# Kernel optimization log

Hardware: AMD Instinct MI355X
Metric: run time of the kernel (lower is better)

Reference implementation:

```python
import jax, jax.numpy as jnp
import numpy as np

C = 64
EPS_LN = 1e-5
EPS_BN = 1e-5


def _conv1x1(x, w, b):
    # x: (B,C,H,W), w: (O,I), b: (O,)
    return jnp.einsum('oi,bihw->bohw', w, x) + b[None, :, None, None]


def _cross_attn(x_a, x_b, wq, bq, wk, bk, wv, bv):
    # query from x_a, key/value from x_b; residual onto x_a
    b, c, h, w = x_a.shape
    hw = h * w
    scale = 1.0 / jnp.sqrt(jnp.asarray(C, x_a.dtype))
    q = _conv1x1(x_a, wq, bq).reshape(b, -1, hw)   # (B,C,HW)
    k = _conv1x1(x_b, wk, bk).reshape(b, -1, hw)   # (B,C,HW)
    v = _conv1x1(x_b, wv, bv).reshape(b, -1, hw)   # (B,C,HW)
    # torch: bmm(k^T, q) -> (B,HW,HW), softmax over last dim
    logits = jnp.einsum('bci,bcj->bij', k, q) * scale
    attn = jax.nn.softmax(logits, axis=-1)
    out = jnp.einsum('bci,bij->bcj', v, attn).reshape(b, -1, h, w)
    return out + x_a


def _layernorm_ch(x, g, b):
    # LayerNorm over channel dim of (B,C,H,W)
    mu = jnp.mean(x, axis=1, keepdims=True)
    var = jnp.var(x, axis=1, keepdims=True)
    xn = (x - mu) * jax.lax.rsqrt(var + EPS_LN)
    return xn * g[None, :, None, None] + b[None, :, None, None]


def setup_inputs() -> dict:
    key = jax.random.key(0)
    ks = jax.random.split(key, 20)
    B, H, W = 4, 64, 64
    s = 0.05
    d = {
        'x_s2': jax.random.normal(ks[0], (B, C, H, W), jnp.float32),
        'x_dem': jax.random.normal(ks[1], (B, C, H, W), jnp.float32),
        'wq1': jax.random.normal(ks[2], (C, C), jnp.float32) * s,
        'bq1': jnp.zeros((C,), jnp.float32),
        'wk1': jax.random.normal(ks[3], (C, C), jnp.float32) * s,
        'bk1': jnp.zeros((C,), jnp.float32),
        'wv1': jax.random.normal(ks[4], (C, C), jnp.float32) * s,
        'bv1': jnp.zeros((C,), jnp.float32),
        'wq2': jax.random.normal(ks[5], (C, C), jnp.float32) * s,
        'bq2': jnp.zeros((C,), jnp.float32),
        'wk2': jax.random.normal(ks[6], (C, C), jnp.float32) * s,
        'bk2': jnp.zeros((C,), jnp.float32),
        'wv2': jax.random.normal(ks[7], (C, C), jnp.float32) * s,
        'bv2': jnp.zeros((C,), jnp.float32),
        'ln_s2_w': jnp.ones((C,), jnp.float32),
        'ln_s2_b': jnp.zeros((C,), jnp.float32),
        'ln_dem_w': jnp.ones((C,), jnp.float32),
        'ln_dem_b': jnp.zeros((C,), jnp.float32),
        'fw1': jax.random.normal(ks[8], (C, 2 * C, 3, 3), jnp.float32) * s,
        'fb1': jnp.zeros((C,), jnp.float32),
        'bn_g': jnp.ones((C,), jnp.float32),
        'bn_b': jnp.zeros((C,), jnp.float32),
        'fw2': jax.random.normal(ks[9], (C, C), jnp.float32) * s,
        'fb2': jnp.zeros((C,), jnp.float32),
    }
    return d


def reference(x_s2, x_dem, wq1, bq1, wk1, bk1, wv1, bv1,
              wq2, bq2, wk2, bk2, wv2, bv2,
              ln_s2_w, ln_s2_b, ln_dem_w, ln_dem_b,
              fw1, fb1, bn_g, bn_b, fw2, fb2):
    out_s2 = _cross_attn(x_s2, x_dem, wq1, bq1, wk1, bk1, wv1, bv1)
    out_dem = _cross_attn(x_dem, x_s2, wq2, bq2, wk2, bk2, wv2, bv2)
    out_s2 = _layernorm_ch(out_s2, ln_s2_w, ln_s2_b)
    out_dem = _layernorm_ch(out_dem, ln_dem_w, ln_dem_b)
    combined = jnp.concatenate([out_s2, out_dem], axis=1)  # (B,2C,H,W)
    y = jax.lax.conv_general_dilated(
        combined, fw1, window_strides=(1, 1), padding='SAME',
        dimension_numbers=('NCHW', 'OIHW', 'NCHW')) + fb1[None, :, None, None]
    # BatchNorm2d in training mode: batch statistics over (B,H,W)
    mu = jnp.mean(y, axis=(0, 2, 3), keepdims=True)
    var = jnp.var(y, axis=(0, 2, 3), keepdims=True)
    y = (y - mu) * jax.lax.rsqrt(var + EPS_BN)
    y = y * bn_g[None, :, None, None] + bn_b[None, :, None, None]
    y = jax.nn.relu(y)
    return _conv1x1(y, fw2, fb2)
```

## Files before the change

### kernel.cpp

```cpp
#include <hip/hip_runtime.h>
#include <hip/hip_bf16.h>


using bf16x8 = __attribute__((ext_vector_type(8))) short;
using f32x4  = __attribute__((ext_vector_type(4))) float;
using f32x16 = __attribute__((ext_vector_type(16))) float;
typedef unsigned int uint2v __attribute__((ext_vector_type(2)));

#define MFMA16(a, b, c) __builtin_amdgcn_mfma_f32_16x16x32_bf16((a), (b), (c), 0, 0, 0)
#define MFMA32(a, b, c) __builtin_amdgcn_mfma_f32_32x32x16_bf16((a), (b), (c), 0, 0, 0)

constexpr int B_ = 4, C_ = 64, S_ = 4096;
constexpr float kQS = 0.18033688f;

constexpr size_t OFF_XT   = 0;
constexpr size_t OFF_WB   = 4u * 1024 * 1024;
constexpr size_t OFF_FW1R = OFF_WB + 64 * 1024;
constexpr size_t OFF_QT   = OFF_FW1R + 160 * 1024;
constexpr size_t OFF_KT   = OFF_QT + 4u * 1024 * 1024;
constexpr size_t OFF_V    = OFF_KT + 4u * 1024 * 1024;
constexpr size_t OFF_COMB = OFF_V + 4u * 1024 * 1024;
constexpr size_t OFF_Y    = OFF_COMB + 4u * 1024 * 1024;
constexpr size_t OFF_PART = OFF_Y + 4u * 1024 * 1024;
constexpr size_t OFF_BNA  = OFF_PART + 512 * 1024;
constexpr size_t OFF_BNB  = OFF_BNA + 1024;

__device__ __forceinline__ unsigned short f2bf(float f) {
  unsigned int u = __float_as_uint(f);
  unsigned int r = (u + 0x7fffu + ((u >> 16) & 1u)) >> 16;
  return (unsigned short)r;
}
__device__ __forceinline__ unsigned int cvt_pk_bf16(float lo, float hi) {
  unsigned int r;
  asm("v_cvt_pk_bf16_f32 %0, %1, %2" : "=v"(r) : "v"(lo), "v"(hi));
  return r;
}
__device__ __forceinline__ float fast_exp2(float x) {
#if __has_builtin(__builtin_amdgcn_exp2f)
  return __builtin_amdgcn_exp2f(x);
#else
  return exp2f(x);
#endif
}
__device__ __forceinline__ void plswap(unsigned int& a, unsigned int& b) {
  uint2v r = __builtin_amdgcn_permlane32_swap(a, b, false, false);
  a = r[0];
  b = r[1];
}

__device__ __forceinline__ void build_pv_frags(const f32x16 s, float& lsum,
                                               bf16x8* out) {
  float p[16];
#pragma unroll
  for (int r = 0; r < 16; ++r) p[r] = fast_exp2(s[r]);
  lsum += (((p[0] + p[1]) + (p[2] + p[3])) + ((p[4] + p[5]) + (p[6] + p[7]))) +
          (((p[8] + p[9]) + (p[10] + p[11])) + ((p[12] + p[13]) + (p[14] + p[15])));
#pragma unroll
  for (int h = 0; h < 2; ++h) {
    unsigned int X  = cvt_pk_bf16(p[8 * h + 0], p[8 * h + 1]);
    unsigned int X2 = cvt_pk_bf16(p[8 * h + 2], p[8 * h + 3]);
    unsigned int Y  = cvt_pk_bf16(p[8 * h + 4], p[8 * h + 5]);
    unsigned int Y2 = cvt_pk_bf16(p[8 * h + 6], p[8 * h + 7]);
    plswap(X, Y);
    plswap(X2, Y2);
    union { unsigned int u[4]; bf16x8 v; } bb;
    bb.u[0] = X; bb.u[1] = X2; bb.u[2] = Y; bb.u[3] = Y2;
    out[h] = bb.v;
  }
}

__global__ void k_prep(const float* wq1, const float* wk1, const float* wv1,
                       const float* wq2, const float* wk2, const float* wv2,
                       const float* fw2, const float* fw1,
                       const float* xs2, const float* xdem,
                       unsigned short* wb, unsigned short* fw1r,
                       unsigned short* xT) {
  __shared__ float lds[64][65];
  if (blockIdx.x < 400) {
    int g = blockIdx.x * 256 + threadIdx.x;
    if (g < 7 * 4096) {
      int m = g >> 12, idx = g & 4095;
      const float* src[7] = {wq1, wk1, wv1, wq2, wk2, wv2, fw2};
      float sc = (m == 0 || m == 3) ? kQS : 1.0f;
      wb[g] = f2bf(src[m][idx] * sc);
    } else {
      int t = g - 7 * 4096;
      if (t < 64 * 1152) {
        int o = t / 1152, kk = t % 1152;
        int dydx = kk >> 7, ci = kk & 127;
        fw1r[t] = f2bf(fw1[o * 1152 + ci * 9 + dydx]);
      }
    }
    return;
  }
  int bid = blockIdx.x - 400;
  int pt = bid & 63, b = (bid >> 6) & 3, tz = bid >> 8;
  int tid = threadIdx.x;
  const float* src = (tz == 0) ? xs2 : xdem;
  int p0 = pt * 64;
#pragma unroll
  for (int k = 0; k < 16; ++k) {
    int idx = k * 256 + tid;
    int c = idx >> 6, pp = idx & 63;
    lds[c][pp] = src[((size_t)(b * 64 + c) << 12) + p0 + pp];
  }
  __syncthreads();
  unsigned short* dst = xT + (size_t)tz * (B_ * S_ * C_);
#pragma unroll
  for (int k = 0; k < 4; ++k) {
    int p = (tid >> 4) + k * 16;
    int c0 = (tid & 15) * 4;
    ushort4 v;
    v.x = f2bf(lds[c0 + 0][p]);
    v.y = f2bf(lds[c0 + 1][p]);
    v.z = f2bf(lds[c0 + 2][p]);
    v.w = f2bf(lds[c0 + 3][p]);
    *(ushort4*)&dst[((size_t)((b << 12) + p0 + p)) * 64 + c0] = v;
  }
}

__global__ __launch_bounds__(256) void k_proj(
    const unsigned short* xT, const unsigned short* wb,
    const float* bq1, const float* bk1, const float* bv1,
    const float* bq2, const float* bk2, const float* bv2,
    unsigned short* Qf, unsigned short* Kf, unsigned short* Vf) {
  int pc = blockIdx.x, b = blockIdx.y, dir = blockIdx.z;
  int lane = threadIdx.x & 63, wid = threadIdx.x >> 6;
  int l4 = lane & 15, g4 = lane >> 4;
  const unsigned short* xq =
      xT + ((size_t)(dir * B_ + b)) * (size_t)(S_ * C_);
  const unsigned short* xkv =
      xT + ((size_t)((1 - dir) * B_ + b)) * (size_t)(S_ * C_);
  size_t dbOff = ((size_t)dir * B_ + b) * (size_t)(S_ * C_);
  const float* bq = dir ? bq2 : bq1;
  const float* bk = dir ? bk2 : bk1;
  const float* bv = dir ? bv2 : bv1;
  int pbase = pc * 64 + wid * 16;

  bf16x8 aq[2], akv[2];
#pragma unroll
  for (int kc = 0; kc < 2; ++kc) {
    aq[kc] = *(const bf16x8*)&xq[(size_t)(pbase + l4) * 64 + kc * 32 + g4 * 8];
    akv[kc] = *(const bf16x8*)&xkv[(size_t)(pbase + l4) * 64 + kc * 32 + g4 * 8];
  }

#pragma unroll
  for (int prod = 0; prod < 2; ++prod) {
    const unsigned short* wm = wb + (dir * 3 + prod) * 4096;
    unsigned short* dst = (prod == 0 ? Qf : Kf) + dbOff;
    const float* bp = (prod == 0) ? bq : bk;
    float bscale = (prod == 0) ? kQS : 1.0f;
    const bf16x8* af = (prod == 0) ? aq : akv;
#pragma unroll
    for (int nt = 0; nt < 4; ++nt) {
      bf16x8 wf0 = *(const bf16x8*)&wm[(nt * 16 + l4) * 64 + g4 * 8];
      bf16x8 wf1 = *(const bf16x8*)&wm[(nt * 16 + l4) * 64 + 32 + g4 * 8];
      f32x4 acc = {0.f, 0.f, 0.f, 0.f};
      acc = MFMA16(af[0], wf0, acc);
      acc = MFMA16(af[1], wf1, acc);
      float bias_c = bp[nt * 16 + l4] * bscale;
#pragma unroll
      for (int r = 0; r < 4; ++r)
        dst[(size_t)nt * 65536 + (size_t)(pbase + g4 * 4 + r) * 16 + l4] =
            f2bf(acc[r] + bias_c);
    }
  }
  {
    const unsigned short* wm = wb + (dir * 3 + 2) * 4096;
    unsigned short* dst = Vf + dbOff;
#pragma unroll
    for (int mt = 0; mt < 4; ++mt) {
      bf16x8 wf0 = *(const bf16x8*)&wm[(mt * 16 + l4) * 64 + g4 * 8];
      bf16x8 wf1 = *(const bf16x8*)&wm[(mt * 16 + l4) * 64 + 32 + g4 * 8];
      f32x4 acc = {0.f, 0.f, 0.f, 0.f};
      acc = MFMA16(wf0, akv[0], acc);
      acc = MFMA16(wf1, akv[1], acc);
#pragma unroll
      for (int r = 0; r < 4; ++r) {
        int c = mt * 16 + g4 * 4 + r;
        dst[(size_t)(pbase >> 4) * 1024 + c * 16 + l4] = f2bf(acc[r] + bv[c]);
      }
    }
  }
}

constexpr int TST = 72;

__global__ __launch_bounds__(256, 2) void k_attn(
    const unsigned short* Qf, const unsigned short* Kf, const unsigned short* Vf,
    const float* xs2, const float* xdem,
    const float* lnw_s2, const float* lnb_s2,
    const float* lnw_dem, const float* lnb_dem,
    unsigned short* comb) {
  __shared__ __align__(16) char smem[34816];
  const f32x16 kZero16 = {0.f, 0.f, 0.f, 0.f, 0.f, 0.f, 0.f, 0.f,
                          0.f, 0.f, 0.f, 0.f, 0.f, 0.f, 0.f, 0.f};
  int bd = blockIdx.x, jb = blockIdx.y;
  int dir = bd >> 2, b = bd & 3;
  int lane = threadIdx.x & 63, wid = threadIdx.x >> 6;
  int l5 = lane & 31;
  int h = lane >> 5;
  int hi8 = h * 8, hi4 = h * 4;
  size_t dbOff = (size_t)bd * (size_t)(S_ * C_);
  const unsigned short* qp = Qf + dbOff;
  const unsigned short* kp = Kf + dbOff;
  const unsigned short* vp = Vf + dbOff;

  int jbase = jb * 64;
  bf16x8 qf[2][4];
#pragma unroll
  for (int jg = 0; jg < 2; ++jg)
#pragma unroll
    for (int kc = 0; kc < 4; ++kc)
      qf[jg][kc] = *(const bf16x8*)&qp[(size_t)kc * 65536 +
                                       (size_t)(jbase + jg * 32 + l5) * 16 + hi8];

  f32x16 acc00 = kZero16, acc01 = kZero16, acc10 = kZero16, acc11 = kZero16;
  float lsum0 = 0.f, lsum1 = 0.f;
  int ibeg = wid * 1024;

#define LOADT(AK, AV, I0)                                                    \
  {                                                                          \
    int i0_ = (I0);                                                          \
    _Pragma("unroll") for (int k_ = 0; k_ < 4; ++k_)                         \
        (AK)[k_] = *(const bf16x8*)&kp[(size_t)k_ * 65536 +                  \
                                       (size_t)(i0_ + l5) * 16 + hi8];       \
    int ic_ = i0_ >> 4;                                                      \
    (AV)[0] = *(const bf16x8*)&vp[(size_t)ic_ * 1024 + l5 * 16 + hi8];       \
    (AV)[1] = *(const bf16x8*)&vp[(size_t)(ic_ + 1) * 1024 + l5 * 16 + hi8]; \
    (AV)[2] = *(const bf16x8*)&vp[(size_t)ic_ * 1024 + (32 + l5) * 16 + hi8];\
    (AV)[3] = *(const bf16x8*)&vp[(size_t)(ic_ + 1) * 1024 + (32 + l5) * 16 + hi8];\
  }

#define TILE(AK, AV)                                                         \
  {                                                                          \
    f32x16 S0 = kZero16;                                                     \
    S0 = MFMA32((AK)[0], qf[0][0], S0);                                      \
    S0 = MFMA32((AK)[1], qf[0][1], S0);                                      \
    S0 = MFMA32((AK)[2], qf[0][2], S0);                                      \
    S0 = MFMA32((AK)[3], qf[0][3], S0);                                      \
    bf16x8 pb0[2];                                                           \
    build_pv_frags(S0, lsum0, pb0);                                          \
    f32x16 S1 = kZero16;                                                     \
    S1 = MFMA32((AK)[0], qf[1][0], S1);                                      \
    S1 = MFMA32((AK)[1], qf[1][1], S1);                                      \
    S1 = MFMA32((AK)[2], qf[1][2], S1);                                      \
    S1 = MFMA32((AK)[3], qf[1][3], S1);                                      \
    bf16x8 pb1[2];                                                           \
    build_pv_frags(S1, lsum1, pb1);                                          \
    acc00 = MFMA32((AV)[0], pb0[0], acc00);                                  \
    acc00 = MFMA32((AV)[1], pb0[1], acc00);                                  \
    acc01 = MFMA32((AV)[2], pb0[0], acc01);                                  \
    acc01 = MFMA32((AV)[3], pb0[1], acc01);                                  \
    acc10 = MFMA32((AV)[0], pb1[0], acc10);                                  \
    acc10 = MFMA32((AV)[1], pb1[1], acc10);                                  \
    acc11 = MFMA32((AV)[2], pb1[0], acc11);                                  \
    acc11 = MFMA32((AV)[3], pb1[1], acc11);                                  \
  }

  bf16x8 akA[4], avA[4], akB[4], avB[4];
  LOADT(akA, avA, ibeg)
  for (int t = 0; t < 32; t += 2) {
    LOADT(akB, avB, ibeg + ((t + 1) & 31) * 32)
    TILE(akA, avA)
    LOADT(akA, avA, ibeg + ((t + 2) & 31) * 32)
    TILE(akB, avB)
  }
#undef LOADT
#undef TILE

  float* Lp = (float*)(smem + 32768);
  Lp[wid * 128 + lane] = lsum0;
  Lp[wid * 128 + 64 + lane] = lsum1;

#define STORE1(A_, CIDX, RG)                                              \
  {                                                                       \
    _Pragma("unroll") for (int q2 = 0; q2 < 4; ++q2) {                    \
      f32x4 tv = {(A_)[q2 * 4 + 0], (A_)[q2 * 4 + 1],                     \
                  (A_)[q2 * 4 + 2], (A_)[q2 * 4 + 3]};                    \
      *(f32x4*)&(RG)[((CIDX) * 4 + q2) * 256 + lane * 4] = tv;            \
    }                                                                     \
  }
#define ADD1(A_, CIDX, RR)                                                \
  {                                                                       \
    _Pragma("unroll") for (int q2 = 0; q2 < 4; ++q2) {                    \
      f32x4 tv = *(const f32x4*)&(RR)[((CIDX) * 4 + q2) * 256 + lane * 4];\
      _Pragma("unroll") for (int e = 0; e < 4; ++e) (A_)[q2 * 4 + e] += tv[e]; \
    }                                                                     \
  }
#define PUB(SLOT)                                                         \
  {                                                                       \
    float* rg_ = (float*)(smem + (size_t)(SLOT) * 16384);                 \
    STORE1(acc00, 0, rg_) STORE1(acc01, 1, rg_)                           \
    STORE1(acc10, 2, rg_) STORE1(acc11, 3, rg_)                           \
  }
#define ADDP(SLOT)                                                        \
  {                                                                       \
    const float* rr_ = (const float*)(smem + (size_t)(SLOT) * 16384);     \
    ADD1(acc00, 0, rr_) ADD1(acc01, 1, rr_)                               \
    ADD1(acc10, 2, rr_) ADD1(acc11, 3, rr_)                               \
  }

  if (wid >= 2) PUB(wid - 2)
  __syncthreads();
  if (wid < 2) ADDP(wid)
  __syncthreads();
  if (wid == 1) PUB(0)
  __syncthreads();
  if (wid != 0) return;
  ADDP(0)
#undef PUB
#undef ADDP
#undef STORE1
#undef ADD1

  const float* xa = (dir == 0 ? xs2 : xdem) + (size_t)b * C_ * S_;
  const float* lw = (dir == 0) ? lnw_s2 : lnw_dem;
  const float* lbp = (dir == 0) ? lnb_s2 : lnb_dem;
  unsigned short* T = (unsigned short*)smem;

#pragma unroll
  for (int jg = 0; jg < 2; ++jg) {
    float ls = 0.f;
#pragma unroll
    for (int w = 0; w < 4; ++w) ls += Lp[w * 128 + jg * 64 + lane];
    ls += __shfl_xor(ls, 32);
    float linv = 1.0f / ls;
    int jcol = jbase + jg * 32 + l5;

    float vals[32];
    float s1 = 0.f, s2 = 0.f;
#pragma unroll
    for (int ct = 0; ct < 2; ++ct)
#pragma unroll
      for (int reg = 0; reg < 16; ++reg) {
        int c = ct * 32 + (reg & 3) + 8 * (reg >> 2) + hi4;
        float a_ = (jg == 0) ? (ct == 0 ? acc00[reg] : acc01[reg])
                             : (ct == 0 ? acc10[reg] : acc11[reg]);
        float v = a_ * linv + xa[(size_t)c * S_ + jcol];
        vals[ct * 16 + reg] = v;
        s1 += v;
        s2 += v * v;
      }
    s1 += __shfl_xor(s1, 32);
    s2 += __shfl_xor(s2, 32);
    float mean = s1 * (1.0f / 64.0f);
    float var = s2 * (1.0f / 64.0f) - mean * mean;
    float rstd = rsqrtf(var + 1e-5f);

#pragma unroll
    for (int ct = 0; ct < 2; ++ct)
#pragma unroll
      for (int q2 = 0; q2 < 4; ++q2)
#pragma unroll
        for (int pp = 0; pp < 2; ++pp) {
          int r0 = q2 * 4 + pp * 2;
          int c0 = ct * 32 + 8 * q2 + hi4 + pp * 2;
          float x0 = (vals[ct * 16 + r0 + 0] - mean) * rstd * lw[c0 + 0] + lbp[c0 + 0];
          float x1 = (vals[ct * 16 + r0 + 1] - mean) * rstd * lw[c0 + 1] + lbp[c0 + 1];
          *(unsigned int*)&T[l5 * TST + c0] = cvt_pk_bf16(x0, x1);
        }
    int j_l = lane >> 1, cc = (lane & 1) * 32;
    unsigned short* cb =
        comb + ((size_t)b * S_ + jbase + jg * 32 + j_l) * 128 + dir * 64 + cc;
    const unsigned short* ts = &T[j_l * TST + cc];
#pragma unroll
    for (int q = 0; q < 4; ++q) {
      uint4 tq = *(const uint4*)&ts[q * 8];
      *(uint4*)&cb[q * 8] = tq;
    }
  }
}

__global__ __launch_bounds__(128) void k_conv3(const unsigned short* comb,
                                               const unsigned short* fw1r,
                                               const float* fb1, float* y,
                                               float* part) {
  int pc = blockIdx.x, b = blockIdx.y;
  int lane = threadIdx.x & 63, wid = threadIdx.x >> 6;
  int l4 = lane & 15, g4 = lane >> 4;
  int p0 = pc * 16;
  int p_l = p0 + l4;
  int py0 = p_l >> 6, px0 = p_l & 63;
  f32x4 acc[2];
#pragma unroll
  for (int o = 0; o < 2; ++o) acc[o] = f32x4{0.f, 0.f, 0.f, 0.f};

#pragma unroll
  for (int kk9 = 0; kk9 < 9; ++kk9) {
    int py = py0 + (kk9 / 3) - 1;
    int px = px0 + (kk9 % 3) - 1;
    bool ok = (py >= 0) && (py < 64) && (px >= 0) && (px < 64);
    const unsigned short* base = comb + ((size_t)(b << 12) + py * 64 + px) * 128;
#pragma unroll
    for (int kc = 0; kc < 4; ++kc) {
      bf16x8 af = {0, 0, 0, 0, 0, 0, 0, 0};
      if (ok) af = *(const bf16x8*)&base[kc * 32 + g4 * 8];
#pragma unroll
      for (int o = 0; o < 2; ++o) {
        int ot = wid * 2 + o;
        bf16x8 bfr = *(const bf16x8*)&fw1r[(size_t)(ot * 16 + l4) * 1152 + kk9 * 128 + kc * 32 + g4 * 8];
        acc[o] = MFMA16(af, bfr, acc[o]);
      }
    }
  }
  int blk = b * 256 + pc;
#pragma unroll
  for (int o = 0; o < 2; ++o) {
    int ot = wid * 2 + o;
    float bias = fb1[ot * 16 + l4];
    float s = 0.f, s2 = 0.f;
#pragma unroll
    for (int r = 0; r < 4; ++r) {
      float v = acc[o][r] + bias;
      y[((size_t)(b << 12) + p0 + g4 * 4 + r) * 64 + ot * 16 + l4] = v;
      s += v;
      s2 += v * v;
    }
    s += __shfl_xor(s, 16);
    s += __shfl_xor(s, 32);
    s2 += __shfl_xor(s2, 16);
    s2 += __shfl_xor(s2, 32);
    if (lane < 16) {
      int ch = ot * 16 + lane;
      part[(size_t)ch * 1024 + blk] = s;
      part[65536 + (size_t)ch * 1024 + blk] = s2;
    }
  }
}

__global__ void k_bnfin(const float* part, const float* bng, const float* bnb,
                        float* bnA, float* bnB) {
  __shared__ float red[2][256];
  int o = blockIdx.x, t = threadIdx.x;
  float s = 0.f, s2 = 0.f;
#pragma unroll
  for (int k = 0; k < 4; ++k) {
    s += part[(size_t)o * 1024 + k * 256 + t];
    s2 += part[65536 + (size_t)o * 1024 + k * 256 + t];
  }
  red[0][t] = s;
  red[1][t] = s2;
  __syncthreads();
#pragma unroll
  for (int off = 128; off >= 1; off >>= 1) {
    if (t < off) {
      red[0][t] += red[0][t + off];
      red[1][t] += red[1][t + off];
    }
    __syncthreads();
  }
  if (t == 0) {
    float mean = red[0][0] * (1.0f / 16384.0f);
    float var = red[1][0] * (1.0f / 16384.0f) - mean * mean;
    float g = bng[o] * rsqrtf(var + 1e-5f);
    bnA[o] = g;
    bnB[o] = bnb[o] - mean * g;
  }
}

__global__ __launch_bounds__(128) void k_final(const float* y, const unsigned short* fw2b,
                                               const float* bnA, const float* bnB,
                                               const float* fb2, float* out) {
  int pc = blockIdx.x, b = blockIdx.y;
  int lane = threadIdx.x & 63, wid = threadIdx.x >> 6;
  int l4 = lane & 15, g4 = lane >> 4;
  int p0 = pc * 16;

  bf16x8 afw[2][2];
#pragma unroll
  for (int m = 0; m < 2; ++m)
#pragma unroll
    for (int kc = 0; kc < 2; ++kc)
      afw[m][kc] = *(const bf16x8*)&fw2b[((wid * 2 + m) * 16 + l4) * 64 + kc * 32 + g4 * 8];
  float a8[2][8], b8[2][8];
#pragma unroll
  for (int kc = 0; kc < 2; ++kc)
#pragma unroll
    for (int e = 0; e < 8; ++e) {
      int c = kc * 32 + g4 * 8 + e;
      a8[kc][e] = bnA[c];
      b8[kc][e] = bnB[c];
    }
  float fbv[2][4];
#pragma unroll
  for (int m = 0; m < 2; ++m)
#pragma unroll
    for (int r = 0; r < 4; ++r) fbv[m][r] = fb2[(wid * 2 + m) * 16 + g4 * 4 + r];

  f32x4 acc[2];
#pragma unroll
  for (int m = 0; m < 2; ++m) acc[m] = f32x4{0.f, 0.f, 0.f, 0.f};

#pragma unroll
  for (int kc = 0; kc < 2; ++kc) {
    const float* yrow = &y[((size_t)(b << 12) + p0 + l4) * 64 + kc * 32 + g4 * 8];
    float4 y0 = *(const float4*)yrow;
    float4 y1 = *(const float4*)(yrow + 4);
    float zv[8] = {y0.x, y0.y, y0.z, y0.w, y1.x, y1.y, y1.z, y1.w};
    bf16x8 zf;
#pragma unroll
    for (int e = 0; e < 8; ++e)
      zf[e] = (short)f2bf(fmaxf(zv[e] * a8[kc][e] + b8[kc][e], 0.f));
#pragma unroll
    for (int m = 0; m < 2; ++m) acc[m] = MFMA16(afw[m][kc], zf, acc[m]);
  }
#pragma unroll
  for (int m = 0; m < 2; ++m)
#pragma unroll
    for (int r = 0; r < 4; ++r)
      out[((size_t)b * 64 + (wid * 2 + m) * 16 + g4 * 4 + r) * (size_t)S_ + p0 + l4] =
          acc[m][r] + fbv[m][r];
}

extern "C" void kernel_launch(void* const* d_in, const int* in_sizes, int n_in,
                              void* d_out, int out_size, void* d_ws, size_t ws_size,
                              hipStream_t stream) {
  const float* x_s2 = (const float*)d_in[0];
  const float* x_dem = (const float*)d_in[1];
  const float* wq1 = (const float*)d_in[2];
  const float* bq1 = (const float*)d_in[3];
  const float* wk1 = (const float*)d_in[4];
  const float* bk1 = (const float*)d_in[5];
  const float* wv1 = (const float*)d_in[6];
  const float* bv1 = (const float*)d_in[7];
  const float* wq2 = (const float*)d_in[8];
  const float* bq2 = (const float*)d_in[9];
  const float* wk2 = (const float*)d_in[10];
  const float* bk2 = (const float*)d_in[11];
  const float* wv2 = (const float*)d_in[12];
  const float* bv2 = (const float*)d_in[13];
  const float* ln_s2_w = (const float*)d_in[14];
  const float* ln_s2_b = (const float*)d_in[15];
  const float* ln_dem_w = (const float*)d_in[16];
  const float* ln_dem_b = (const float*)d_in[17];
  const float* fw1 = (const float*)d_in[18];
  const float* fb1 = (const float*)d_in[19];
  const float* bn_g = (const float*)d_in[20];
  const float* bn_b = (const float*)d_in[21];
  const float* fw2 = (const float*)d_in[22];
  const float* fb2 = (const float*)d_in[23];

  char* ws = (char*)d_ws;
  unsigned short* xT = (unsigned short*)(ws + OFF_XT);
  unsigned short* wbuf = (unsigned short*)(ws + OFF_WB);
  unsigned short* fw1r = (unsigned short*)(ws + OFF_FW1R);
  unsigned short* Qf = (unsigned short*)(ws + OFF_QT);
  unsigned short* Kf = (unsigned short*)(ws + OFF_KT);
  unsigned short* Vf = (unsigned short*)(ws + OFF_V);
  unsigned short* comb = (unsigned short*)(ws + OFF_COMB);
  float* ybuf = (float*)(ws + OFF_Y);
  float* part = (float*)(ws + OFF_PART);
  float* bnA = (float*)(ws + OFF_BNA);
  float* bnB = (float*)(ws + OFF_BNB);

  k_prep<<<912, 256, 0, stream>>>(wq1, wk1, wv1, wq2, wk2, wv2, fw2, fw1,
                                  x_s2, x_dem, wbuf, fw1r, xT);
  k_proj<<<dim3(64, 4, 2), 256, 0, stream>>>(xT, wbuf, bq1, bk1, bv1,
                                             bq2, bk2, bv2, Qf, Kf, Vf);
  k_attn<<<dim3(8, 64), 256, 0, stream>>>(Qf, Kf, Vf, x_s2, x_dem,
                                          ln_s2_w, ln_s2_b, ln_dem_w, ln_dem_b,
                                          comb);
  k_conv3<<<dim3(256, 4), 128, 0, stream>>>(comb, fw1r, fb1, ybuf, part);
  k_bnfin<<<64, 256, 0, stream>>>(part, bn_g, bn_b, bnA, bnB);
  k_final<<<dim3(256, 4), 128, 0, stream>>>(ybuf, wbuf + 6 * 4096, bnA, bnB, fb2,
                                            (float*)d_out);
}
```

Before: 92.00 us.

## Split attention key range across two blocks with atomic-flag merge

Doubles the attention grid by splitting the key/value range in half across a new grid z dimension. Each block writes its partial accumulators and row sums to global scratch, then bumps a per-tile atomic counter, and the second block to finish merges both halves and runs the layernorm epilogue. This aims to raise occupancy and parallelism on a grid of only 512 blocks. The cost is extra global traffic for the partials, fences, and flag resets in the prep kernel.

```diff
diff --git a/kernel.cpp b/kernel.cpp
--- a/kernel.cpp
+++ b/kernel.cpp
@@ -21,9 +21,12 @@
 constexpr size_t OFF_V    = OFF_KT + 4u * 1024 * 1024;
 constexpr size_t OFF_COMB = OFF_V + 4u * 1024 * 1024;
 constexpr size_t OFF_Y    = OFF_COMB + 4u * 1024 * 1024;
+constexpr size_t OFF_PACC = OFF_Y;
 constexpr size_t OFF_PART = OFF_Y + 4u * 1024 * 1024;
 constexpr size_t OFF_BNA  = OFF_PART + 512 * 1024;
 constexpr size_t OFF_BNB  = OFF_BNA + 1024;
+constexpr size_t OFF_PL   = OFF_Y + 16u * 1024 * 1024;
+constexpr size_t OFF_FLAG = OFF_PL + 256 * 1024;
 
 __device__ __forceinline__ unsigned short f2bf(float f) {
   unsigned int u = __float_as_uint(f);
@@ -74,10 +77,14 @@
                        const float* fw2, const float* fw1,
                        const float* xs2, const float* xdem,
                        unsigned short* wb, unsigned short* fw1r,
-                       unsigned short* xT) {
+                       unsigned short* xT, int* flags) {
   __shared__ float lds[64][65];
   if (blockIdx.x < 400) {
     int g = blockIdx.x * 256 + threadIdx.x;
+    if (blockIdx.x == 0) {
+      flags[threadIdx.x] = 0;
+      flags[256 + threadIdx.x] = 0;
+    }
     if (g < 7 * 4096) {
       int m = g >> 12, idx = g & 4095;
       const float* src[7] = {wq1, wk1, wv1, wq2, wk2, wv2, fw2};
@@ -191,11 +198,11 @@
     const float* xs2, const float* xdem,
     const float* lnw_s2, const float* lnb_s2,
     const float* lnw_dem, const float* lnb_dem,
-    unsigned short* comb) {
+    unsigned short* comb, float* pacc, float* pl, int* flags) {
   __shared__ __align__(16) char smem[34816];
   const f32x16 kZero16 = {0.f, 0.f, 0.f, 0.f, 0.f, 0.f, 0.f, 0.f,
                           0.f, 0.f, 0.f, 0.f, 0.f, 0.f, 0.f, 0.f};
-  int bd = blockIdx.x, jb = blockIdx.y;
+  int bd = blockIdx.x, jb = blockIdx.y, ihz = blockIdx.z;
   int dir = bd >> 2, b = bd & 3;
   int lane = threadIdx.x & 63, wid = threadIdx.x >> 6;
   int l5 = lane & 31;
@@ -217,7 +224,7 @@
 
   f32x16 acc00 = kZero16, acc01 = kZero16, acc10 = kZero16, acc11 = kZero16;
   float lsum0 = 0.f, lsum1 = 0.f;
-  int ibeg = wid * 1024;
+  int ibeg = ihz * 2048 + wid * 512;
 
 #define LOADT(AK, AV, I0)                                                    \
   {                                                                          \
@@ -260,10 +267,10 @@
 
   bf16x8 akA[4], avA[4], akB[4], avB[4];
   LOADT(akA, avA, ibeg)
-  for (int t = 0; t < 32; t += 2) {
-    LOADT(akB, avB, ibeg + ((t + 1) & 31) * 32)
+  for (int t = 0; t < 16; t += 2) {
+    LOADT(akB, avB, ibeg + ((t + 1) & 15) * 32)
     TILE(akA, avA)
-    LOADT(akA, avA, ibeg + ((t + 2) & 31) * 32)
+    LOADT(akA, avA, ibeg + ((t + 2) & 15) * 32)
     TILE(akB, avB)
   }
 #undef LOADT
@@ -309,6 +316,37 @@
   __syncthreads();
   if (wid != 0) return;
   ADDP(0)
+
+  float lsA[2];
+#pragma unroll
+  for (int jg = 0; jg < 2; ++jg) {
+    float ls = 0.f;
+#pragma unroll
+    for (int w = 0; w < 4; ++w) ls += Lp[w * 128 + jg * 64 + lane];
+    ls += __shfl_xor(ls, 32);
+    lsA[jg] = ls;
+  }
+
+  int pidx = bd * 64 + jb;
+  float* pme = pacc + ((size_t)pidx * 2 + ihz) * 4096;
+  STORE1(acc00, 0, pme) STORE1(acc01, 1, pme)
+  STORE1(acc10, 2, pme) STORE1(acc11, 3, pme)
+  if (lane < 32) {
+    pl[((size_t)pidx * 2 + ihz) * 64 + lane] = lsA[0];
+    pl[((size_t)pidx * 2 + ihz) * 64 + 32 + lane] = lsA[1];
+  }
+  __threadfence();
+  int old = 0;
+  if (lane == 0) old = atomicAdd(&flags[pidx], 1);
+  old = __shfl(old, 0);
+  if (old == 0) return;
+  __threadfence();
+
+  const float* po = pacc + ((size_t)pidx * 2 + (1 - ihz)) * 4096;
+  ADDP_G: ;
+  ADD1(acc00, 0, po) ADD1(acc01, 1, po)
+  ADD1(acc10, 2, po) ADD1(acc11, 3, po)
+  const float* plo = pl + ((size_t)pidx * 2 + (1 - ihz)) * 64;
 #undef PUB
 #undef ADDP
 #undef STORE1
@@ -321,10 +359,7 @@
 
 #pragma unroll
   for (int jg = 0; jg < 2; ++jg) {
-    float ls = 0.f;
-#pragma unroll
-    for (int w = 0; w < 4; ++w) ls += Lp[w * 128 + jg * 64 + lane];
-    ls += __shfl_xor(ls, 32);
+    float ls = lsA[jg] + plo[jg * 32 + l5];
     float linv = 1.0f / ls;
     int jcol = jbase + jg * 32 + l5;
 
@@ -550,17 +585,20 @@
   unsigned short* Vf = (unsigned short*)(ws + OFF_V);
   unsigned short* comb = (unsigned short*)(ws + OFF_COMB);
   float* ybuf = (float*)(ws + OFF_Y);
+  float* pacc = (float*)(ws + OFF_PACC);
+  float* plbuf = (float*)(ws + OFF_PL);
+  int* flags = (int*)(ws + OFF_FLAG);
   float* part = (float*)(ws + OFF_PART);
   float* bnA = (float*)(ws + OFF_BNA);
   float* bnB = (float*)(ws + OFF_BNB);
 
   k_prep<<<912, 256, 0, stream>>>(wq1, wk1, wv1, wq2, wk2, wv2, fw2, fw1,
-                                  x_s2, x_dem, wbuf, fw1r, xT);
+                                  x_s2, x_dem, wbuf, fw1r, xT, flags);
   k_proj<<<dim3(64, 4, 2), 256, 0, stream>>>(xT, wbuf, bq1, bk1, bv1,
                                              bq2, bk2, bv2, Qf, Kf, Vf);
-  k_attn<<<dim3(8, 64), 256, 0, stream>>>(Qf, Kf, Vf, x_s2, x_dem,
-                                          ln_s2_w, ln_s2_b, ln_dem_w, ln_dem_b,
-                                          comb);
+  k_attn<<<dim3(8, 64, 2), 256, 0, stream>>>(Qf, Kf, Vf, x_s2, x_dem,
+                                             ln_s2_w, ln_s2_b, ln_dem_w, ln_dem_b,
+                                             comb, pacc, plbuf, flags);
   k_conv3<<<dim3(256, 4), 128, 0, stream>>>(comb, fw1r, fb1, ybuf, part);
   k_bnfin<<<64, 256, 0, stream>>>(part, bn_g, bn_b, bnA, bnB);
   k_final<<<dim3(256, 4), 128, 0, stream>>>(ybuf, wbuf + 6 * 4096, bnA, bnB, fb2,
```

Result: slower. 141.5 us (+53.8%).
